# Performance work log

Measured on AMD Instinct MI355X. Metric: run time of the kernel, lower is better.

Reference implementation:

```python
import jax, jax.numpy as jnp
import numpy as np

ALPHA_MIN = 1e-6
TAU_EPS = 1e-3


def _spectral_normalize(W):
    # spectral_norm divides by the largest singular value of W
    sigma = jnp.linalg.svd(W, compute_uv=False)[0]
    return W / sigma


def setup_inputs() -> dict:
    key = jax.random.key(0)
    ks = jax.random.split(key, 10)
    B, T, D, k = 8, 8192, 128, 64
    x = jax.random.normal(ks[0], (B, T, D), dtype=jnp.float32)
    dt = jax.random.uniform(ks[1], (B, T), dtype=jnp.float32) * (2.0 / T)
    alpha_mod = 0.1 * jax.random.normal(ks[2], (B, T, k), dtype=jnp.float32)
    omega_mod = 0.1 * jax.random.normal(ks[3], (B, T, k), dtype=jnp.float32)
    tau_mod = 0.1 * jax.random.normal(ks[4], (B, T, 1), dtype=jnp.float32)
    s_real_raw = jax.random.normal(ks[5], (k,), dtype=jnp.float32)
    s_imag = jax.random.uniform(ks[6], (k,), dtype=jnp.float32, minval=-np.pi, maxval=np.pi)
    tau_raw = jnp.zeros((), dtype=jnp.float32)
    W = jax.random.normal(ks[7], (k, D), dtype=jnp.float32) * (1.0 / np.sqrt(D))
    b = jax.random.uniform(ks[8], (k,), dtype=jnp.float32, minval=-1.0 / np.sqrt(D), maxval=1.0 / np.sqrt(D))
    return {"x": x, "dt": dt, "alpha_mod": alpha_mod, "omega_mod": omega_mod,
            "tau_mod": tau_mod, "s_real_raw": s_real_raw, "s_imag": s_imag,
            "tau_raw": tau_raw, "W": W, "b": b}


def reference(x, dt, alpha_mod, omega_mod, tau_mod, s_real_raw, s_imag, tau_raw, W, b):
    # recurrent mode of LearnableLaplacianBasis
    B, T, D = x.shape
    k = s_imag.shape[0]
    W_sn = _spectral_normalize(W)
    u = jnp.einsum('btd,kd->btk', x, W_sn) + b  # [B,T,k]

    tau = jax.nn.softplus(tau_raw) + TAU_EPS
    alpha0 = (jax.nn.softplus(s_real_raw) + ALPHA_MIN) * tau  # [k]
    omega0 = s_imag * tau                                      # [k]

    alpha = alpha0 * jnp.exp(alpha_mod)   # [B,T,k]
    omega = omega0 * jnp.exp(omega_mod)
    scale = jnp.exp(tau_mod)              # [B,T,1] broadcasts to [B,T,k]
    alpha = alpha * scale
    omega = omega * scale

    dt_bt1 = dt[:, :, None]
    rho = jnp.exp(-alpha * dt_bt1)
    theta = omega * dt_bt1
    cos_t = jnp.cos(theta)
    sin_t = jnp.sin(theta)

    # time-major for scan: [T,B,k]
    xs = (jnp.swapaxes(rho, 0, 1), jnp.swapaxes(cos_t, 0, 1),
          jnp.swapaxes(sin_t, 0, 1), jnp.swapaxes(u, 0, 1))

    def step(carry, inp):
        c, s = carry
        r, ct, st, ut = inp
        c2 = r * (c * ct - s * st) + ut
        s2 = r * (c * st + s * ct)
        return (c2, s2), (c2, s2)

    init = (jnp.zeros((B, k), x.dtype), jnp.zeros((B, k), x.dtype))
    _, (C, S) = jax.lax.scan(step, init, xs)  # [T,B,k] each
    C = jnp.swapaxes(C, 0, 1)
    S = jnp.swapaxes(S, 0, 1)
    return jnp.concatenate([C, S], axis=2)  # [B,T,2k]
```

## Files before the change

kernel.cpp:

```cpp
#include <hip/hip_runtime.h>
#include <hip/hip_bf16.h>

#define B_   8
#define T_   8192
#define D_   128
#define K_   64
#define TC   16
#define NC   512
#define SEG  16
#define NSEG 32

#define GEMM_BLOCKS 1024
#define GP 136

typedef float  floatx4  __attribute__((ext_vector_type(4)));
typedef __bf16 bf16x8   __attribute__((ext_vector_type(8)));
typedef unsigned short ushortx8 __attribute__((ext_vector_type(8)));

__device__ inline unsigned short f2bf(float f) {
  unsigned u = __float_as_uint(f);
  u = u + 0x7FFFu + ((u >> 16) & 1u);
  return (unsigned short)(u >> 16);
}
__device__ inline float bf2f(unsigned short h) {
  return __uint_as_float(((unsigned)h) << 16);
}

#define MP 72

__global__ __launch_bounds__(256) void k_gemm_sigma(
    const float* __restrict__ x, const float* __restrict__ W,
    float* __restrict__ V, float* __restrict__ sig) {
  __shared__ __align__(16) unsigned char smem[2 * 64 * GP * 2 + 512];

  const int tid  = threadIdx.x;
  const int lane = tid & 63;
  const int wv   = tid >> 6;
  const int l15  = lane & 15;
  const int q    = lane >> 4;

  if (blockIdx.x == GEMM_BLOCKS) {
    unsigned short* Ma = (unsigned short*)smem;
    unsigned short* Mb = Ma + 64 * MP;
    float* red = (float*)(smem + 2 * 64 * MP * 2);
    float* vsh = red + 4;
    int*   jsh = (int*)(vsh + 64);

    floatx4 acc[4] = {};
    const int arow = 16 * wv + l15;
    for (int s = 0; s < 4; ++s) {
      const int kb = 32 * s + 8 * q;
      float4 a0 = *(const float4*)(W + arow * 128 + kb);
      float4 a1 = *(const float4*)(W + arow * 128 + kb + 4);
      ushortx8 ua;
      ua[0] = f2bf(a0.x); ua[1] = f2bf(a0.y); ua[2] = f2bf(a0.z); ua[3] = f2bf(a0.w);
      ua[4] = f2bf(a1.x); ua[5] = f2bf(a1.y); ua[6] = f2bf(a1.z); ua[7] = f2bf(a1.w);
      bf16x8 av = __builtin_bit_cast(bf16x8, ua);
      for (int tn = 0; tn < 4; ++tn) {
        const int brow = 16 * tn + l15;
        float4 b0 = *(const float4*)(W + brow * 128 + kb);
        float4 b1 = *(const float4*)(W + brow * 128 + kb + 4);
        ushortx8 ub;
        ub[0] = f2bf(b0.x); ub[1] = f2bf(b0.y); ub[2] = f2bf(b0.z); ub[3] = f2bf(b0.w);
        ub[4] = f2bf(b1.x); ub[5] = f2bf(b1.y); ub[6] = f2bf(b1.z); ub[7] = f2bf(b1.w);
        bf16x8 bv = __builtin_bit_cast(bf16x8, ub);
        acc[tn] = __builtin_amdgcn_mfma_f32_16x16x32_bf16(av, bv, acc[tn], 0, 0, 0);
      }
    }
    float mx = 0.f;
    for (int tn = 0; tn < 4; ++tn)
      for (int r = 0; r < 4; ++r) mx = fmaxf(mx, fabsf(acc[tn][r]));
    for (int off = 32; off; off >>= 1) mx = fmaxf(mx, __shfl_xor(mx, off));
    if (lane == 0) red[wv] = mx;
    __syncthreads();
    {
      float gm  = fmaxf(fmaxf(red[0], red[1]), fmaxf(red[2], red[3]));
      float inv = 1.f / gm;
      for (int tn = 0; tn < 4; ++tn)
        for (int r = 0; r < 4; ++r)
          Ma[(16 * wv + 4 * q + r) * MP + 16 * tn + l15] = f2bf(acc[tn][r] * inv);
    }
    __syncthreads();

    unsigned short* src = Ma;
    unsigned short* dst = Mb;
    for (int it = 0; it < 8; ++it) {
      floatx4 f[4] = {};
      for (int s = 0; s < 2; ++s) {
        const int kb = 32 * s + 8 * q;
        uint4 ua4 = *(const uint4*)(src + (16 * wv + l15) * MP + kb);
        bf16x8 av = __builtin_bit_cast(bf16x8, ua4);
        for (int tn = 0; tn < 4; ++tn) {
          const int n = 16 * tn + l15;
          ushortx8 ub;
          #pragma unroll
          for (int j = 0; j < 8; ++j) ub[j] = src[(kb + j) * MP + n];
          bf16x8 bv = __builtin_bit_cast(bf16x8, ub);
          f[tn] = __builtin_amdgcn_mfma_f32_16x16x32_bf16(av, bv, f[tn], 0, 0, 0);
        }
      }
      float m2 = 0.f;
      for (int tn = 0; tn < 4; ++tn)
        for (int r = 0; r < 4; ++r) m2 = fmaxf(m2, fabsf(f[tn][r]));
      for (int off = 32; off; off >>= 1) m2 = fmaxf(m2, __shfl_xor(m2, off));
      if (lane == 0) red[wv] = m2;
      __syncthreads();
      {
        float gm2  = fmaxf(fmaxf(red[0], red[1]), fmaxf(red[2], red[3]));
        float inv2 = 1.f / gm2;
        for (int tn = 0; tn < 4; ++tn)
          for (int r = 0; r < 4; ++r)
            dst[(16 * wv + 4 * q + r) * MP + 16 * tn + l15] = f2bf(f[tn][r] * inv2);
      }
      __syncthreads();
      unsigned short* t2 = src; src = dst; dst = t2;
    }

    if (tid == 0) {
      int jb = 0; float best = -1.f;
      for (int j = 0; j < 64; ++j) {
        float dv = bf2f(src[j * MP + j]);
        if (dv > best) { best = dv; jb = j; }
      }
      *jsh = jb;
    }
    __syncthreads();
    if (tid < 64) vsh[tid] = bf2f(src[tid * MP + *jsh]);
    __syncthreads();

    if (wv == 0) {
      float wa = 0.f, wb = 0.f;
      for (int i = 0; i < 64; ++i) {
        float vi = vsh[i];
        wa = fmaf(W[i * 128 + lane], vi, wa);
        wb = fmaf(W[i * 128 + 64 + lane], vi, wb);
      }
      float num = wa * wa + wb * wb;
      float den = vsh[lane] * vsh[lane];
      for (int off = 32; off; off >>= 1) {
        num += __shfl_xor(num, off);
        den += __shfl_xor(den, off);
      }
      if (lane == 0) sig[0] = 1.f / sqrtf(num / den);
    }
    return;
  }

  unsigned short* Wh = (unsigned short*)smem;
  unsigned short* Wl = Wh + 64 * GP;

  #pragma unroll
  for (int j = 0; j < 8; ++j) {
    const int v = tid + 256 * j;
    float4 w4 = ((const float4*)W)[v];
    const int e = v * 4;
    const int row = e >> 7, col = e & 127;
    float a[4] = {w4.x, w4.y, w4.z, w4.w};
    unsigned short h[4], l[4];
    #pragma unroll
    for (int i = 0; i < 4; ++i) {
      h[i] = f2bf(a[i]);
      l[i] = f2bf(a[i] - bf2f(h[i]));
    }
    unsigned hp0 = (unsigned)h[0] | ((unsigned)h[1] << 16);
    unsigned hp1 = (unsigned)h[2] | ((unsigned)h[3] << 16);
    unsigned lp0 = (unsigned)l[0] | ((unsigned)l[1] << 16);
    unsigned lp1 = (unsigned)l[2] | ((unsigned)l[3] << 16);
    *(uint2*)(Wh + row * GP + col) = make_uint2(hp0, hp1);
    *(uint2*)(Wl + row * GP + col) = make_uint2(lp0, lp1);
  }
  __syncthreads();

  const int R0 = blockIdx.x * 64 + wv * 16;
  floatx4 acc[4] = {};

  #pragma unroll
  for (int s = 0; s < 4; ++s) {
    const float* xp = x + ((size_t)(R0 + l15) << 7) + 32 * s + 8 * q;
    float4 x0 = *(const float4*)xp;
    float4 x1 = *(const float4*)(xp + 4);
    float xs8[8] = {x0.x, x0.y, x0.z, x0.w, x1.x, x1.y, x1.z, x1.w};
    ushortx8 uh, ul;
    #pragma unroll
    for (int j = 0; j < 8; ++j) {
      unsigned short h = f2bf(xs8[j]);
      uh[j] = h;
      ul[j] = f2bf(xs8[j] - bf2f(h));
    }
    bf16x8 ah = __builtin_bit_cast(bf16x8, uh);
    bf16x8 al = __builtin_bit_cast(bf16x8, ul);

    #pragma unroll
    for (int t = 0; t < 4; ++t) {
      const unsigned short* bp = Wh + (16 * t + l15) * GP + 32 * s + 8 * q;
      bf16x8 bh = __builtin_bit_cast(bf16x8, *(const uint4*)bp);
      const unsigned short* bq = Wl + (16 * t + l15) * GP + 32 * s + 8 * q;
      bf16x8 bl = __builtin_bit_cast(bf16x8, *(const uint4*)bq);
      acc[t] = __builtin_amdgcn_mfma_f32_16x16x32_bf16(ah, bh, acc[t], 0, 0, 0);
      acc[t] = __builtin_amdgcn_mfma_f32_16x16x32_bf16(al, bh, acc[t], 0, 0, 0);
      acc[t] = __builtin_amdgcn_mfma_f32_16x16x32_bf16(ah, bl, acc[t], 0, 0, 0);
    }
  }

  #pragma unroll
  for (int t = 0; t < 4; ++t)
    #pragma unroll
    for (int r = 0; r < 4; ++r)
      V[(size_t)(R0 + 4 * q + r) * 64 + 16 * t + l15] = acc[t][r];
}

#define STEP_PREP()                                                     \
    float alpha = alpha0 * __expf(a_ + tmv);                            \
    float omega = omega0 * __expf(o_ + tmv);                            \
    float rho = __expf(-alpha * dtv);                                   \
    float th  = omega * dtv;                                            \
    float th2 = th * th;                                                \
    float st  = th * fmaf(th2, -0.16666667f, 1.f);                      \
    float ct  = fmaf(th2, -0.5f, 1.f);                                  \
    float ar  = rho * ct, ai = rho * st;

__global__ __launch_bounds__(256) void k_phaseA(
    const float* __restrict__ am, const float* __restrict__ om,
    const float* __restrict__ tm, const float* __restrict__ dtp,
    const float* __restrict__ V,  const float* __restrict__ sr,
    const float* __restrict__ si, const float* __restrict__ traw,
    const float* __restrict__ bb, const float* __restrict__ sig,
    float* __restrict__ T4) {
  const int lane = threadIdx.x & 63;
  const int wgl  = __builtin_amdgcn_readfirstlane(blockIdx.x * 4 + (threadIdx.x >> 6));
  const int b = wgl >> 9;
  const int c = wgl & (NC - 1);
  const float tau    = log1pf(__expf(traw[0])) + 1e-3f;
  const float alpha0 = (log1pf(__expf(sr[lane])) + 1e-6f) * tau;
  const float omega0 = si[lane] * tau;
  const float bk     = bb[lane];
  const float invs   = sig[0];
  const int bt0 = b * T_ + c * TC;
  size_t base = (size_t)bt0 * 64 + lane;
  float Ar = 1.f, Ai = 0.f, Ur = 0.f, Ui = 0.f;
  #pragma unroll 4
  for (int t = 0; t < TC; ++t) {
    float a_  = am[base];
    float o_  = om[base];
    float v_  = V[base];
    float tmv = tm[bt0 + t];
    float dtv = dtp[bt0 + t];
    STEP_PREP();
    float u   = fmaf(v_, invs, bk);
    float nUr = fmaf(ar, Ur, fmaf(-ai, Ui, u));
    float nUi = fmaf(ar, Ui, ai * Ur);
    Ur = nUr; Ui = nUi;
    float nAr = fmaf(ar, Ar, -ai * Ai);
    float nAi = fmaf(ar, Ai, ai * Ar);
    Ar = nAr; Ai = nAi;
    base += 64;
  }
  *(float4*)(T4 + (size_t)(c * 512 + b * 64 + lane) * 4) = make_float4(Ar, Ai, Ur, Ui);
}

__global__ __launch_bounds__(256) void k_segagg(const float* __restrict__ T4,
                                                float* __restrict__ SA) {
  const int t = blockIdx.x * 256 + threadIdx.x;
  const int g = t >> 9;
  const int s = t & 511;
  float Ar = 1.f, Ai = 0.f, Ur = 0.f, Ui = 0.f;
  for (int i = 0; i < SEG; ++i) {
    const int c = g * SEG + i;
    float4 tr = *(const float4*)(T4 + (size_t)(c * 512 + s) * 4);
    float nUr = tr.x * Ur - tr.y * Ui + tr.z;
    float nUi = tr.x * Ui + tr.y * Ur + tr.w;
    float nAr = tr.x * Ar - tr.y * Ai;
    float nAi = tr.x * Ai + tr.y * Ar;
    Ar = nAr; Ai = nAi; Ur = nUr; Ui = nUi;
  }
  *(float4*)(SA + (size_t)t * 4) = make_float4(Ar, Ai, Ur, Ui);
}

__global__ __launch_bounds__(64) void k_segscan(const float* __restrict__ SA,
                                                const float* __restrict__ T4,
                                                float* __restrict__ Z0) {
  __shared__ float sz[NSEG * 2];
  const int s   = blockIdx.x;
  const int tid = threadIdx.x;
  if (tid == 0) {
    float zr = 0.f, zi = 0.f;
    #pragma unroll
    for (int g = 0; g < NSEG; ++g) {
      sz[2 * g] = zr; sz[2 * g + 1] = zi;
      float4 a = *(const float4*)(SA + (size_t)(g * 512 + s) * 4);
      float nr = a.x * zr - a.y * zi + a.z;
      float ni = a.x * zi + a.y * zr + a.w;
      zr = nr; zi = ni;
    }
  }
  __syncthreads();
  if (tid < NSEG) {
    float zr = sz[2 * tid], zi = sz[2 * tid + 1];
    for (int i = 0; i < SEG; ++i) {
      const int c = tid * SEG + i;
      const size_t o = (size_t)(c * 512 + s);
      Z0[o * 2] = zr; Z0[o * 2 + 1] = zi;
      float4 a = *(const float4*)(T4 + o * 4);
      float nr = a.x * zr - a.y * zi + a.z;
      float ni = a.x * zi + a.y * zr + a.w;
      zr = nr; zi = ni;
    }
  }
}

__global__ __launch_bounds__(256) void k_phaseC(
    const float* __restrict__ am, const float* __restrict__ om,
    const float* __restrict__ tm, const float* __restrict__ dtp,
    const float* __restrict__ V,  const float* __restrict__ sr,
    const float* __restrict__ si, const float* __restrict__ traw,
    const float* __restrict__ bb, const float* __restrict__ sig,
    const float* __restrict__ Z0, float* __restrict__ out) {
  const int lane = threadIdx.x & 63;
  const int wgl  = __builtin_amdgcn_readfirstlane(blockIdx.x * 4 + (threadIdx.x >> 6));
  const int b = wgl >> 9;
  const int c = wgl & (NC - 1);
  const float tau    = log1pf(__expf(traw[0])) + 1e-3f;
  const float alpha0 = (log1pf(__expf(sr[lane])) + 1e-6f) * tau;
  const float omega0 = si[lane] * tau;
  const float bk     = bb[lane];
  const float invs   = sig[0];
  const size_t zo = (size_t)(c * 512 + b * 64 + lane) * 2;
  float zr = Z0[zo], zi = Z0[zo + 1];
  const int bt0 = b * T_ + c * TC;
  size_t base = (size_t)bt0 * 64 + lane;
  float* outp = out + (size_t)bt0 * 128 + lane;
  #pragma unroll 4
  for (int t = 0; t < TC; ++t) {
    float a_  = am[base];
    float o_  = om[base];
    float v_  = V[base];
    float tmv = tm[bt0 + t];
    float dtv = dtp[bt0 + t];
    STEP_PREP();
    float u  = fmaf(v_, invs, bk);
    float nr = fmaf(ar, zr, fmaf(-ai, zi, u));
    float ni = fmaf(ar, zi, ai * zr);
    zr = nr; zi = ni;
    outp[0]  = zr;
    outp[64] = zi;
    base += 64; outp += 128;
  }
}

extern "C" void kernel_launch(void* const* d_in, const int* in_sizes, int n_in,
                              void* d_out, int out_size, void* d_ws, size_t ws_size,
                              hipStream_t stream) {
  (void)in_sizes; (void)n_in; (void)out_size; (void)ws_size;
  const float* x    = (const float*)d_in[0];
  const float* dtp  = (const float*)d_in[1];
  const float* amod = (const float*)d_in[2];
  const float* omod = (const float*)d_in[3];
  const float* tmod = (const float*)d_in[4];
  const float* srr  = (const float*)d_in[5];
  const float* sim  = (const float*)d_in[6];
  const float* traw = (const float*)d_in[7];
  const float* W    = (const float*)d_in[8];
  const float* bb   = (const float*)d_in[9];
  float* out = (float*)d_out;
  float* ws  = (float*)d_ws;

  float* sig = ws;
  float* V   = ws + 16;
  float* T4  = V  + (size_t)B_ * T_ * K_;
  float* SA  = T4 + (size_t)NC * 512 * 4;
  float* Z0  = SA + (size_t)NSEG * 512 * 4;

  k_gemm_sigma<<<GEMM_BLOCKS + 1, 256, 0, stream>>>(x, W, V, sig);
  k_phaseA <<<1024, 256, 0, stream>>>(amod, omod, tmod, dtp, V, srr, sim, traw, bb, sig, T4);
  k_segagg <<<NSEG * 2, 256, 0, stream>>>(T4, SA);
  k_segscan<<<512, 64,  0, stream>>>(SA, T4, Z0);
  k_phaseC <<<1024, 256, 0, stream>>>(amod, omod, tmod, dtp, V, srr, sim, traw, bb, sig, Z0, out);
}
```

Measured before the change: 167.2 us.

## Fuse chunked scan phases into single-pass kernel with decoupled block lookback

Replaces the four scan kernels (local aggregate, segment aggregate, segment scan, output pass) with one kernel of 1024-thread blocks. Each block combines its 16 wave chunks through shared memory, publishes its block aggregate with a flag, and waits on earlier blocks in the same batch. Per-step coefficients are kept in registers, so the second pass no longer rereads alpha_mod, omega_mod and V or recomputes the exponentials. This removes three kernel launches and about half the input traffic. In exchange it adds inter-block spin-waiting, which relies on all 256 blocks being co-resident (or dispatched in order) to avoid deadlock, plus extra register pressure.

```diff
diff --git a/kernel.cpp b/kernel.cpp
--- a/kernel.cpp
+++ b/kernel.cpp
@@ -6,9 +6,6 @@
 #define D_   128
 #define K_   64
 #define TC   16
-#define NC   512
-#define SEG  16
-#define NSEG 32
 
 #define GEMM_BLOCKS 1024
 #define GP 136
@@ -30,7 +27,7 @@
 
 __global__ __launch_bounds__(256) void k_gemm_sigma(
     const float* __restrict__ x, const float* __restrict__ W,
-    float* __restrict__ V, float* __restrict__ sig) {
+    float* __restrict__ V, float* __restrict__ sig, int* __restrict__ FL) {
   __shared__ __align__(16) unsigned char smem[2 * 64 * GP * 2 + 512];
 
   const int tid  = threadIdx.x;
@@ -40,6 +37,8 @@
   const int q    = lane >> 4;
 
   if (blockIdx.x == GEMM_BLOCKS) {
+    FL[tid] = 0;
+
     unsigned short* Ma = (unsigned short*)smem;
     unsigned short* Mb = Ma + 64 * MP;
     float* red = (float*)(smem + 2 * 64 * MP * 2);
@@ -219,26 +218,36 @@
     float ct  = fmaf(th2, -0.5f, 1.f);                                  \
     float ar  = rho * ct, ai = rho * st;
 
-__global__ __launch_bounds__(256) void k_phaseA(
+__global__ __launch_bounds__(1024, 8) void k_fused(
     const float* __restrict__ am, const float* __restrict__ om,
     const float* __restrict__ tm, const float* __restrict__ dtp,
     const float* __restrict__ V,  const float* __restrict__ sr,
     const float* __restrict__ si, const float* __restrict__ traw,
     const float* __restrict__ bb, const float* __restrict__ sig,
-    float* __restrict__ T4) {
-  const int lane = threadIdx.x & 63;
-  const int wgl  = __builtin_amdgcn_readfirstlane(blockIdx.x * 4 + (threadIdx.x >> 6));
-  const int b = wgl >> 9;
-  const int c = wgl & (NC - 1);
+    float* __restrict__ BA, int* __restrict__ FL,
+    float* __restrict__ out) {
+  __shared__ float4 sAgg[16 * 64];
+
+  const int tid  = threadIdx.x;
+  const int lane = tid & 63;
+  const int w    = __builtin_amdgcn_readfirstlane(tid >> 6);
+  const int g    = blockIdx.x;
+  const int b    = g >> 5;
+  const int tb   = g & 31;
+  const int gb   = g & ~31;
+
   const float tau    = log1pf(__expf(traw[0])) + 1e-3f;
   const float alpha0 = (log1pf(__expf(sr[lane])) + 1e-6f) * tau;
   const float omega0 = si[lane] * tau;
   const float bk     = bb[lane];
   const float invs   = sig[0];
-  const int bt0 = b * T_ + c * TC;
+
+  const int bt0 = b * T_ + tb * 256 + w * TC;
   size_t base = (size_t)bt0 * 64 + lane;
+
+  float car[TC], cai[TC], cu[TC];
   float Ar = 1.f, Ai = 0.f, Ur = 0.f, Ui = 0.f;
-  #pragma unroll 4
+  #pragma unroll
   for (int t = 0; t < TC; ++t) {
     float a_  = am[base];
     float o_  = om[base];
@@ -246,7 +255,8 @@
     float tmv = tm[bt0 + t];
     float dtv = dtp[bt0 + t];
     STEP_PREP();
-    float u   = fmaf(v_, invs, bk);
+    float u = fmaf(v_, invs, bk);
+    car[t] = ar; cai[t] = ai; cu[t] = u;
     float nUr = fmaf(ar, Ur, fmaf(-ai, Ui, u));
     float nUi = fmaf(ar, Ui, ai * Ur);
     Ur = nUr; Ui = nUi;
@@ -255,95 +265,58 @@
     Ar = nAr; Ai = nAi;
     base += 64;
   }
-  *(float4*)(T4 + (size_t)(c * 512 + b * 64 + lane) * 4) = make_float4(Ar, Ai, Ur, Ui);
-}
-
-__global__ __launch_bounds__(256) void k_segagg(const float* __restrict__ T4,
-                                                float* __restrict__ SA) {
-  const int t = blockIdx.x * 256 + threadIdx.x;
-  const int g = t >> 9;
-  const int s = t & 511;
-  float Ar = 1.f, Ai = 0.f, Ur = 0.f, Ui = 0.f;
-  for (int i = 0; i < SEG; ++i) {
-    const int c = g * SEG + i;
-    float4 tr = *(const float4*)(T4 + (size_t)(c * 512 + s) * 4);
-    float nUr = tr.x * Ur - tr.y * Ui + tr.z;
-    float nUi = tr.x * Ui + tr.y * Ur + tr.w;
-    float nAr = tr.x * Ar - tr.y * Ai;
-    float nAi = tr.x * Ai + tr.y * Ar;
-    Ar = nAr; Ai = nAi; Ur = nUr; Ui = nUi;
-  }
-  *(float4*)(SA + (size_t)t * 4) = make_float4(Ar, Ai, Ur, Ui);
-}
-
-__global__ __launch_bounds__(64) void k_segscan(const float* __restrict__ SA,
-                                                const float* __restrict__ T4,
-                                                float* __restrict__ Z0) {
-  __shared__ float sz[NSEG * 2];
-  const int s   = blockIdx.x;
-  const int tid = threadIdx.x;
-  if (tid == 0) {
-    float zr = 0.f, zi = 0.f;
-    #pragma unroll
-    for (int g = 0; g < NSEG; ++g) {
-      sz[2 * g] = zr; sz[2 * g + 1] = zi;
-      float4 a = *(const float4*)(SA + (size_t)(g * 512 + s) * 4);
-      float nr = a.x * zr - a.y * zi + a.z;
-      float ni = a.x * zi + a.y * zr + a.w;
-      zr = nr; zi = ni;
-    }
-  }
+  sAgg[w * 64 + lane] = make_float4(Ar, Ai, Ur, Ui);
   __syncthreads();
-  if (tid < NSEG) {
-    float zr = sz[2 * tid], zi = sz[2 * tid + 1];
-    for (int i = 0; i < SEG; ++i) {
-      const int c = tid * SEG + i;
-      const size_t o = (size_t)(c * 512 + s);
-      Z0[o * 2] = zr; Z0[o * 2 + 1] = zi;
-      float4 a = *(const float4*)(T4 + o * 4);
-      float nr = a.x * zr - a.y * zi + a.z;
-      float ni = a.x * zi + a.y * zr + a.w;
-      zr = nr; zi = ni;
-    }
-  }
-}
-
-__global__ __launch_bounds__(256) void k_phaseC(
-    const float* __restrict__ am, const float* __restrict__ om,
-    const float* __restrict__ tm, const float* __restrict__ dtp,
-    const float* __restrict__ V,  const float* __restrict__ sr,
-    const float* __restrict__ si, const float* __restrict__ traw,
-    const float* __restrict__ bb, const float* __restrict__ sig,
-    const float* __restrict__ Z0, float* __restrict__ out) {
-  const int lane = threadIdx.x & 63;
-  const int wgl  = __builtin_amdgcn_readfirstlane(blockIdx.x * 4 + (threadIdx.x >> 6));
-  const int b = wgl >> 9;
-  const int c = wgl & (NC - 1);
-  const float tau    = log1pf(__expf(traw[0])) + 1e-3f;
-  const float alpha0 = (log1pf(__expf(sr[lane])) + 1e-6f) * tau;
-  const float omega0 = si[lane] * tau;
-  const float bk     = bb[lane];
-  const float invs   = sig[0];
-  const size_t zo = (size_t)(c * 512 + b * 64 + lane) * 2;
-  float zr = Z0[zo], zi = Z0[zo + 1];
-  const int bt0 = b * T_ + c * TC;
-  size_t base = (size_t)bt0 * 64 + lane;
+
+  float Er = 1.f, Ei = 0.f, Fr = 0.f, Fi = 0.f;
+  for (int j = 0; j < w; ++j) {
+    float4 a = sAgg[j * 64 + lane];
+    float nEr = a.x * Er - a.y * Ei;
+    float nEi = a.x * Ei + a.y * Er;
+    float nFr = fmaf(a.x, Fr, fmaf(-a.y, Fi, a.z));
+    float nFi = fmaf(a.x, Fi, fmaf(a.y, Fr, a.w));
+    Er = nEr; Ei = nEi; Fr = nFr; Fi = nFi;
+  }
+
+  if (w == 15) {
+    float bAr = Ar * Er - Ai * Ei;
+    float bAi = Ar * Ei + Ai * Er;
+    float bUr = fmaf(Ar, Fr, fmaf(-Ai, Fi, Ur));
+    float bUi = fmaf(Ar, Fi, fmaf(Ai, Fr, Ui));
+    *(float4*)(BA + (size_t)(g * 64 + lane) * 4) = make_float4(bAr, bAi, bUr, bUi);
+    __threadfence();
+  }
+  __syncthreads();
+  if (tid == 0)
+    __hip_atomic_store(&FL[g], 1, __ATOMIC_RELEASE, __HIP_MEMORY_SCOPE_AGENT);
+
+  if (tid < tb) {
+    while (__hip_atomic_load(&FL[gb + tid], __ATOMIC_ACQUIRE,
+                             __HIP_MEMORY_SCOPE_AGENT) == 0)
+      __builtin_amdgcn_s_sleep(2);
+  }
+  __syncthreads();
+  __threadfence();
+
+  float Hr = 0.f, Hi = 0.f;
+  for (int j = 0; j < tb; ++j) {
+    float4 a = *(const float4*)(BA + (size_t)((gb + j) * 64 + lane) * 4);
+    float nHr = fmaf(a.x, Hr, fmaf(-a.y, Hi, a.z));
+    float nHi = fmaf(a.x, Hi, fmaf(a.y, Hr, a.w));
+    Hr = nHr; Hi = nHi;
+  }
+  float zr = fmaf(Er, Hr, fmaf(-Ei, Hi, Fr));
+  float zi = fmaf(Er, Hi, fmaf(Ei, Hr, Fi));
+
   float* outp = out + (size_t)bt0 * 128 + lane;
-  #pragma unroll 4
+  #pragma unroll
   for (int t = 0; t < TC; ++t) {
-    float a_  = am[base];
-    float o_  = om[base];
-    float v_  = V[base];
-    float tmv = tm[bt0 + t];
-    float dtv = dtp[bt0 + t];
-    STEP_PREP();
-    float u  = fmaf(v_, invs, bk);
-    float nr = fmaf(ar, zr, fmaf(-ai, zi, u));
-    float ni = fmaf(ar, zi, ai * zr);
+    float nr = fmaf(car[t], zr, fmaf(-cai[t], zi, cu[t]));
+    float ni = fmaf(car[t], zi, cai[t] * zr);
     zr = nr; zi = ni;
     outp[0]  = zr;
     outp[64] = zi;
-    base += 64; outp += 128;
+    outp += 128;
   }
 }
 
@@ -366,13 +339,10 @@
 
   float* sig = ws;
   float* V   = ws + 16;
-  float* T4  = V  + (size_t)B_ * T_ * K_;
-  float* SA  = T4 + (size_t)NC * 512 * 4;
-  float* Z0  = SA + (size_t)NSEG * 512 * 4;
-
-  k_gemm_sigma<<<GEMM_BLOCKS + 1, 256, 0, stream>>>(x, W, V, sig);
-  k_phaseA <<<1024, 256, 0, stream>>>(amod, omod, tmod, dtp, V, srr, sim, traw, bb, sig, T4);
-  k_segagg <<<NSEG * 2, 256, 0, stream>>>(T4, SA);
-  k_segscan<<<512, 64,  0, stream>>>(SA, T4, Z0);
-  k_phaseC <<<1024, 256, 0, stream>>>(amod, omod, tmod, dtp, V, srr, sim, traw, bb, sig, Z0, out);
-}
+  float* BA  = V + (size_t)B_ * T_ * K_;
+  int*   FL  = (int*)(BA + 256 * 64 * 4);
+
+  k_gemm_sigma<<<GEMM_BLOCKS + 1, 256, 0, stream>>>(x, W, V, sig, FL);
+  k_fused<<<256, 1024, 0, stream>>>(amod, omod, tmod, dtp, V, srr, sim, traw,
+                                    bb, sig, BA, FL, out);
+}
```

New measurement: 232.9 us. 39.2% more time.
